# Kernel optimization log

Hardware: AMD Instinct MI355X
Metric: run time of the kernel (lower is better)

## Reference

```python
import jax, jax.numpy as jnp
import numpy as np

B, L, D, H, K = 4, 4096, 1024, 16, 256

def setup_inputs() -> dict:
    key = jax.random.key(0)
    ks = jax.random.split(key, 11)
    s = 0.02
    return {
        "x": jax.random.normal(ks[0], (B, L, D), jnp.float32),
        "Wq": jax.random.normal(ks[1], (D, D), jnp.float32) * s,
        "bq": jax.random.normal(ks[2], (D,), jnp.float32) * s,
        "Wk": jax.random.normal(ks[3], (D, D), jnp.float32) * s,
        "bk": jax.random.normal(ks[4], (D,), jnp.float32) * s,
        "Wv": jax.random.normal(ks[5], (D, D), jnp.float32) * s,
        "bv": jax.random.normal(ks[6], (D,), jnp.float32) * s,
        "E": jax.random.normal(ks[7], (L, K), jnp.float32),
        "F": jax.random.normal(ks[8], (L, K), jnp.float32),
        "Wo": jax.random.normal(ks[9], (D, D), jnp.float32) * s,
        "bo": jax.random.normal(ks[10], (D,), jnp.float32) * s,
        "n_heads": H,
    }

def reference(x, Wq, bq, Wk, bk, Wv, bv, E, F, Wo, bo, n_heads):
    Bc, Lc, Dc = x.shape
    hd = Dc // n_heads
    scale = hd ** -0.5
    # QKV projections (torch Linear: x @ W.T + b; here W stored as [in,out])
    q = (x @ Wq + bq).reshape(Bc, Lc, n_heads, hd)  # blhd
    k = (x @ Wk + bk).reshape(Bc, Lc, n_heads, hd)
    v = (x @ Wv + bv).reshape(Bc, Lc, n_heads, hd)
    # Low-rank projection of K/V sequence dim: L -> K
    kE = jnp.einsum('blhd,lk->bhkd', k, E[:Lc])
    vF = jnp.einsum('blhd,lk->bhkd', v, F[:Lc])
    # Attention over compressed dim k
    qk = jnp.einsum('blhd,bhkd->bhlk', q, kE) * scale
    attn = jax.nn.softmax(qk, axis=-1)
    out = jnp.einsum('bhlk,bhkd->blhd', attn, vF).reshape(Bc, Lc, Dc)
    return out @ Wo + bo
```

## Files before the change

kernel.cpp:

```cpp
#include <hip/hip_runtime.h>

typedef _Float16 half_t;
typedef __attribute__((ext_vector_type(8))) _Float16 f16x8;
typedef __attribute__((ext_vector_type(4))) _Float16 f16x4;
typedef __attribute__((ext_vector_type(4))) float f32x4;
typedef __attribute__((ext_vector_type(4))) float float4v;

__device__ __forceinline__ void gload_lds16(const void* g, void* l) {
  __builtin_amdgcn_global_load_lds(
      (const __attribute__((address_space(1))) void*)g,
      (__attribute__((address_space(3))) void*)l, 16, 0, 0);
}

template<int OUTMODE>
__global__ __launch_bounds__(512, 2)
void gemm_big(const half_t* __restrict__ A, const half_t* __restrict__ Bt,
              void* __restrict__ Cv, const float* __restrict__ bias, float alpha)
{
  __shared__ __attribute__((aligned(16))) char lds[131072];
  const int tid = threadIdx.x, w = tid >> 6, lane = tid & 63;
  const int wr = w >> 2, wc = w & 3;
  const int g = lane >> 4, cc = lane & 15;
  const int m0 = blockIdx.x * 256, n0 = blockIdx.y * 256;

  const int srow2 = tid >> 2, sslot = tid & 3;
  const int swslot = sslot ^ ((srow2 >> 1) & 3);
  const int swr = (g ^ ((cc >> 1) & 3)) << 4;

  const f32x4 zero = {0.f, 0.f, 0.f, 0.f};
  f32x4 acc[8][4];
#pragma unroll
  for (int i = 0; i < 8; ++i)
#pragma unroll
    for (int j = 0; j < 4; ++j) acc[i][j] = zero;

  auto STAGE_HALF = [&](int ktile, int hh, char* sb) {
    const int kk = hh >> 1, isB = hh & 1;
    const half_t* src = isB ? Bt : A;
    const int base_row = isB ? n0 : m0;
    const long rowoff = (long)(base_row + srow2) * 1024 + ktile * 64 + kk * 32 + swslot * 8;
    char* d = sb + isB * 32768 + kk * 16384;
    gload_lds16(src + rowoff,          d + tid * 16);
    gload_lds16(src + rowoff + 131072, d + 8192 + tid * 16);
  };

  {
    char* b0 = lds;
    STAGE_HALF(0, 0, b0); STAGE_HALF(0, 1, b0);
    STAGE_HALF(0, 2, b0); STAGE_HALF(0, 3, b0);
  }
  asm volatile("s_waitcnt vmcnt(4)" ::: "memory");
  __builtin_amdgcn_s_barrier();

#pragma unroll 1
  for (int n = 0; n < 16; ++n) {
    const char* rb = lds + ((n & 1) << 16);
    char* sb = lds + (((n + 1) & 1) << 16);
    f16x8 bf[4];
#pragma unroll
    for (int ph = 0; ph < 4; ++ph) {
      const int kk = ph >> 1, fh = ph & 1;
      f16x8 af[4];
      const char* Ah = rb + kk * 16384;
#pragma unroll
      for (int mf = 0; mf < 4; ++mf)
        af[mf] = *(const f16x8*)(Ah + (wr * 128 + fh * 64 + mf * 16 + cc) * 64 + swr);
      if (fh == 0) {
        const char* Bh = rb + 32768 + kk * 16384;
#pragma unroll
        for (int nf = 0; nf < 4; ++nf)
          bf[nf] = *(const f16x8*)(Bh + (wc * 64 + nf * 16 + cc) * 64 + swr);
      }
      if (n < 15) STAGE_HALF(n + 1, ph, sb);
      __builtin_amdgcn_sched_barrier(0);
      __builtin_amdgcn_s_barrier();
      asm volatile("s_waitcnt lgkmcnt(0)" ::: "memory");
      __builtin_amdgcn_sched_barrier(0);
      __builtin_amdgcn_s_setprio(1);
#pragma unroll
      for (int mf = 0; mf < 4; ++mf)
#pragma unroll
        for (int nf = 0; nf < 4; ++nf)
          acc[fh * 4 + mf][nf] =
              __builtin_amdgcn_mfma_f32_16x16x32_f16(af[mf], bf[nf], acc[fh * 4 + mf][nf], 0, 0, 0);
      __builtin_amdgcn_s_setprio(0);
      __builtin_amdgcn_sched_barrier(0);
      if (ph == 1) {
        if (n < 15) { asm volatile("s_waitcnt vmcnt(4)" ::: "memory"); }
        else        { asm volatile("s_waitcnt vmcnt(0)" ::: "memory"); }
      } else if (ph == 3) {
        if (n < 15) { asm volatile("s_waitcnt vmcnt(4)" ::: "memory"); }
      }
      __builtin_amdgcn_s_barrier();
    }
  }

#pragma unroll
  for (int mf = 0; mf < 8; ++mf)
#pragma unroll
    for (int nf = 0; nf < 4; ++nf)
#pragma unroll
      for (int r = 0; r < 4; ++r) {
        const int row = m0 + wr * 128 + mf * 16 + g * 4 + r;
        const int col = n0 + wc * 64 + nf * 16 + cc;
        float v = (acc[mf][nf][r] + bias[col]) * alpha;
        if (OUTMODE == 0) {
          ((float*)Cv)[(long)row * 1024 + col] = v;
        } else if (OUTMODE == 1) {
          ((half_t*)Cv)[(long)row * 1024 + col] = (half_t)v;
        } else {
          const int bb = row >> 12, l = row & 4095, h = col >> 6, d = col & 63;
          ((half_t*)Cv)[(((long)(bb * 16 + h) * 4096 + l) << 6) + d] = (half_t)v;
        }
      }
}

template<int BM, int BN, int WM, int WN, int OUTF16, int MODE, int SK>
__global__ __launch_bounds__(256, 2)
void gemm_bt(const half_t* __restrict__ A, const half_t* __restrict__ Bt,
             void* __restrict__ Cv, const float* __restrict__ bias,
             const float* __restrict__ rowscale,
             int M, int N, int K, int lda, int ldb, int ldc, float alpha,
             long sA, long sB, long sC)
{
  constexpr int FM = WM / 16, FN = WN / 16, CW = BN / WN;
  __shared__ __attribute__((aligned(16))) half_t As[BM * 32];
  __shared__ __attribute__((aligned(16))) half_t Bs[BN * 32];

  const int tid = threadIdx.x, w = tid >> 6, lane = tid & 63;
  const int wr = w / CW, wc = w % CW;
  const int z = blockIdx.z / SK, ks = blockIdx.z % SK;
  const half_t* Ab = A + (long)z * sA;
  const half_t* Bb = Bt + (long)z * sB;
  const int m0 = blockIdx.x * BM, n0 = blockIdx.y * BN;
  const int g = lane >> 4, cc = lane & 15;
  const int srow = lane >> 2, scol = (lane & 3) * 8;

  const f32x4 zero = {0.f, 0.f, 0.f, 0.f};
  f32x4 acc[FM][FN];
#pragma unroll
  for (int i = 0; i < FM; ++i)
#pragma unroll
    for (int j = 0; j < FN; ++j) acc[i][j] = zero;

  const int kchunk = K / SK;
  for (int kt = ks * kchunk; kt < (ks + 1) * kchunk; kt += 32) {
#pragma unroll
    for (int j = 0; j < BM / 64; ++j) {
      const int bi = w * (BM / 64) + j;
      gload_lds16(Ab + (long)(m0 + bi * 16 + srow) * lda + kt + scol, &As[bi * 512]);
    }
#pragma unroll
    for (int j = 0; j < BN / 64; ++j) {
      const int bi = w * (BN / 64) + j;
      gload_lds16(Bb + (long)(n0 + bi * 16 + srow) * ldb + kt + scol, &Bs[bi * 512]);
    }
    __syncthreads();

    f16x8 af[FM], bf[FN];
#pragma unroll
    for (int i = 0; i < FM; ++i)
      af[i] = *(const f16x8*)&As[(wr * WM + i * 16 + cc) * 32 + g * 8];
#pragma unroll
    for (int j = 0; j < FN; ++j)
      bf[j] = *(const f16x8*)&Bs[(wc * WN + j * 16 + cc) * 32 + g * 8];
#pragma unroll
    for (int i = 0; i < FM; ++i)
#pragma unroll
      for (int j = 0; j < FN; ++j)
        acc[i][j] = __builtin_amdgcn_mfma_f32_16x16x32_f16(af[i], bf[j], acc[i][j], 0, 0, 0);
    __syncthreads();
  }

  const long coff = (long)z * sC;
#pragma unroll
  for (int i = 0; i < FM; ++i)
#pragma unroll
    for (int j = 0; j < FN; ++j)
#pragma unroll
      for (int r = 0; r < 4; ++r) {
        const int row = m0 + wr * WM + i * 16 + g * 4 + r;
        const int col = n0 + wc * WN + j * 16 + cc;
        float v = acc[i][j][r];
        if (MODE == 1) v = (v + bias[col]) * alpha;
        if (MODE == 2 || MODE == 4) v = v + rowscale[row] * bias[col];
        if (MODE == 3) {
          const int nb = gridDim.z / SK;
          ((float*)Cv)[((long)ks * nb + z) * sC + (long)row * ldc + col] = v;
        } else if (MODE == 4) {
          ((half_t*)Cv)[coff + (long)(col >> 6) * ((long)M * 64) + (long)row * 64 + (col & 63)]
              = (half_t)v;
        } else {
          if (OUTF16) ((half_t*)Cv)[coff + (long)row * ldc + col] = (half_t)v;
          else        ((float*)Cv)[coff + (long)row * ldc + col] = v;
        }
      }
}

__global__ __launch_bounds__(512, 2)
void attn_fused(const half_t* __restrict__ qhb, const half_t* __restrict__ kEh,
                const half_t* __restrict__ vFt, half_t* __restrict__ outp, int L)
{
  __shared__ __attribute__((aligned(16))) half_t Ks[256 * 64];
  __shared__ __attribute__((aligned(16))) half_t Vs[64 * 256];
  const int tid = threadIdx.x, w = tid >> 6, lane = tid & 63;
  const int g = lane >> 4, c = lane & 15;
  const int l0 = blockIdx.x * 256, h = blockIdx.y, b = blockIdx.z;

  const half_t* keh = kEh + (long)(b * 16 + h) * 16384;
  const half_t* vfh = vFt + (long)b * 262144 + (long)h * 16384;
  const half_t* qpan = qhb + ((long)(b * 16 + h) * 4096 + l0) * 64;
  half_t* ob = outp + ((long)b * L + l0 + w * 32) * 1024 + h * 64;

#pragma unroll
  for (int i = 0; i < 4; ++i) {
    const int row = i * 64 + (tid >> 3), slot = tid & 7;
    gload_lds16(qpan + row * 64 + ((slot ^ (row & 7)) << 3),
                (char*)Ks + i * 8192 + tid * 16);
  }
  __syncthreads();

  f16x8 qf[2][2];
#pragma unroll
  for (int fi = 0; fi < 2; ++fi) {
    const int qrow = w * 32 + fi * 16 + c;
    const char* qp = (const char*)Ks + qrow * 128;
#pragma unroll
    for (int ks = 0; ks < 2; ++ks)
      qf[fi][ks] = *(const f16x8*)(qp + (((ks * 4 + g) ^ (qrow & 7)) << 4));
  }
  __syncthreads();

#pragma unroll
  for (int i = 0; i < 4; ++i) {
    const int row = i * 64 + (tid >> 3), slot = tid & 7;
    gload_lds16(keh + row * 64 + ((slot ^ (row & 7)) << 3),
                (char*)Ks + i * 8192 + tid * 16);
  }
#pragma unroll
  for (int i = 0; i < 4; ++i) {
    const int row = i * 16 + (tid >> 5), slot = tid & 31;
    gload_lds16(vfh + row * 256 + ((slot ^ (row & 7)) << 3),
                (char*)Vs + i * 8192 + tid * 16);
  }
  __syncthreads();

  const f32x4 zero = {0.f, 0.f, 0.f, 0.f};
  f32x4 o[2][4];
#pragma unroll
  for (int fi = 0; fi < 2; ++fi)
#pragma unroll
    for (int fd = 0; fd < 4; ++fd) o[fi][fd] = zero;
  float mrun[2] = {-3.0e38f, -3.0e38f};
  float lrun[2] = {0.f, 0.f};

  for (int ch = 0; ch < 4; ++ch) {
    f32x4 s[2][4];
#pragma unroll
    for (int fi = 0; fi < 2; ++fi)
#pragma unroll
      for (int fj = 0; fj < 4; ++fj) s[fi][fj] = zero;
#pragma unroll
    for (int fj = 0; fj < 4; ++fj) {
      const int krow = ch * 64 + fj * 16 + c;
      const char* kb = (const char*)Ks + krow * 128;
      f16x8 k0 = *(const f16x8*)(kb + ((g ^ (c & 7)) << 4));
      f16x8 k1 = *(const f16x8*)(kb + (((4 + g) ^ (c & 7)) << 4));
#pragma unroll
      for (int fi = 0; fi < 2; ++fi) {
        s[fi][fj] = __builtin_amdgcn_mfma_f32_16x16x32_f16(k0, qf[fi][0], s[fi][fj], 0, 0, 0);
        s[fi][fj] = __builtin_amdgcn_mfma_f32_16x16x32_f16(k1, qf[fi][1], s[fi][fj], 0, 0, 0);
      }
    }

    f16x4 p[2][4];
#pragma unroll
    for (int fi = 0; fi < 2; ++fi) {
      float cm = -3.0e38f;
#pragma unroll
      for (int fj = 0; fj < 4; ++fj)
#pragma unroll
        for (int r = 0; r < 4; ++r) cm = fmaxf(cm, s[fi][fj][r]);
      cm = fmaxf(cm, __shfl_xor(cm, 16));
      cm = fmaxf(cm, __shfl_xor(cm, 32));
      const float mnew = fmaxf(mrun[fi], cm);
      const float sc = __expf(mrun[fi] - mnew);
      float csum = 0.f;
#pragma unroll
      for (int fj = 0; fj < 4; ++fj) {
        f16x4 fr;
#pragma unroll
        for (int r = 0; r < 4; ++r) {
          float e = __expf(s[fi][fj][r] - mnew);
          fr[r] = (half_t)e; csum += e;
        }
        p[fi][fj] = fr;
      }
      csum += __shfl_xor(csum, 16);
      csum += __shfl_xor(csum, 32);
      lrun[fi] = lrun[fi] * sc + csum;
      mrun[fi] = mnew;
#pragma unroll
      for (int fd = 0; fd < 4; ++fd)
#pragma unroll
        for (int r = 0; r < 4; ++r) o[fi][fd][r] *= sc;
    }

#pragma unroll
    for (int kc = 0; kc < 4; ++kc) {
      const int s16 = ch * 8 + kc * 2 + (g >> 1);
      f16x4 va[4];
#pragma unroll
      for (int fd = 0; fd < 4; ++fd) {
        const int drow = fd * 16 + c;
        va[fd] = *(const f16x4*)((const char*)Vs + drow * 512 +
                                 ((s16 ^ (c & 7)) << 4) + (g & 1) * 8);
      }
#pragma unroll
      for (int fi = 0; fi < 2; ++fi)
#pragma unroll
        for (int fd = 0; fd < 4; ++fd)
          o[fi][fd] = __builtin_amdgcn_mfma_f32_16x16x16f16(va[fd], p[fi][kc], o[fi][fd], 0, 0, 0);
    }
  }

#pragma unroll
  for (int fi = 0; fi < 2; ++fi) {
    const float inv = 1.0f / lrun[fi];
#pragma unroll
    for (int fd = 0; fd < 4; ++fd) {
      f16x4 st;
#pragma unroll
      for (int r = 0; r < 4; ++r) st[r] = (half_t)(o[fi][fd][r] * inv);
      *(f16x4*)(ob + (long)(fi * 16 + c) * 1024 + fd * 16 + g * 4) = st;
    }
  }
}

__global__ void reduce4_f16(const float* __restrict__ in, half_t* __restrict__ out) {
  long i = ((long)blockIdx.x * 256 + threadIdx.x) * 4;
  float4v a = *(const float4v*)(in + i);
#pragma unroll
  for (int ks = 1; ks < 4; ++ks) {
    float4v t = *(const float4v*)(in + (long)ks * 2097152 + i);
    a.x += t.x; a.y += t.y; a.z += t.z; a.w += t.w;
  }
  f16x4 o;
  o[0] = (half_t)a.x; o[1] = (half_t)a.y; o[2] = (half_t)a.z; o[3] = (half_t)a.w;
  *(f16x4*)(out + i) = o;
}

__global__ void xpass(const float* __restrict__ x, half_t* __restrict__ xhf,
                      half_t* __restrict__ xT) {
  __shared__ float t[32][33];
  const int b = blockIdx.z, d0 = blockIdx.x * 32, l0 = blockIdx.y * 32;
  const int tx = threadIdx.x, ty = threadIdx.y;
  const float* ip = x + ((long)b * 4096 + l0) * 1024 + d0;
  half_t* oh = xhf + ((long)b * 4096 + l0) * 1024 + d0;
#pragma unroll
  for (int j = 0; j < 4; ++j) {
    float v = ip[(long)(ty + 8 * j) * 1024 + tx];
    t[ty + 8 * j][tx] = v;
    oh[(long)(ty + 8 * j) * 1024 + tx] = (half_t)v;
  }
  __syncthreads();
  half_t* ot = xT + ((long)b * 1024 + d0) * 4096 + l0;
#pragma unroll
  for (int j = 0; j < 4; ++j)
    ot[(long)(ty + 8 * j) * 4096 + tx] = (half_t)t[tx][ty + 8 * j];
}

__global__ void efpass(const float* __restrict__ E, const float* __restrict__ F,
                       half_t* __restrict__ outT, float* __restrict__ ssum) {
  __shared__ float t[32][33];
  __shared__ float ps[8][32];
  const int zz = blockIdx.z;
  const float* in = zz ? F : E;
  half_t* oT = outT + (long)zz * 1048576;
  float* sm = ssum + zz * 256;
  const int k0 = blockIdx.x * 32, l0 = blockIdx.y * 32;
  const int tx = threadIdx.x, ty = threadIdx.y;
  float p = 0.f;
#pragma unroll
  for (int j = 0; j < 4; ++j) {
    float v = in[(long)(l0 + ty + 8 * j) * 256 + k0 + tx];
    t[ty + 8 * j][tx] = v; p += v;
  }
  ps[ty][tx] = p;
  __syncthreads();
  if (ty == 0) {
    float a = 0.f;
#pragma unroll
    for (int r = 0; r < 8; ++r) a += ps[r][tx];
    atomicAdd(&sm[k0 + tx], a);
  }
#pragma unroll
  for (int j = 0; j < 4; ++j)
    oT[(long)(k0 + ty + 8 * j) * 4096 + l0 + tx] = (half_t)t[tx][ty + 8 * j];
}

__global__ void transposeW(const float* __restrict__ W0, const float* __restrict__ W1,
                           const float* __restrict__ W2, const float* __restrict__ W3,
                           half_t* __restrict__ out0, half_t* __restrict__ out1,
                           half_t* __restrict__ out2, half_t* __restrict__ out3) {
  __shared__ float t[32][33];
  const int zz = blockIdx.z;
  const float* in = (zz == 0) ? W0 : (zz == 1) ? W1 : (zz == 2) ? W2 : W3;
  half_t* out = (zz == 0) ? out0 : (zz == 1) ? out1 : (zz == 2) ? out2 : out3;
  const int cx = blockIdx.x * 32 + threadIdx.x;
  const int r0 = blockIdx.y * 32;
#pragma unroll
  for (int j = 0; j < 4; ++j)
    t[threadIdx.y + 8 * j][threadIdx.x] = in[(long)(r0 + threadIdx.y + 8 * j) * 1024 + cx];
  __syncthreads();
  const int rx = r0 + threadIdx.x;
  const int cy = blockIdx.x * 32 + threadIdx.y;
#pragma unroll
  for (int j = 0; j < 4; ++j)
    out[(long)(cy + 8 * j) * 1024 + rx] = (half_t)t[threadIdx.x][threadIdx.y + 8 * j];
}

extern "C" void kernel_launch(void* const* d_in, const int* in_sizes, int n_in,
                              void* d_out, int out_size, void* d_ws, size_t ws_size,
                              hipStream_t stream)
{
  const float* x  = (const float*)d_in[0];
  const float* Wq = (const float*)d_in[1];
  const float* bq = (const float*)d_in[2];
  const float* Wk = (const float*)d_in[3];
  const float* bk = (const float*)d_in[4];
  const float* Wv = (const float*)d_in[5];
  const float* bv = (const float*)d_in[6];
  const float* E  = (const float*)d_in[7];
  const float* F  = (const float*)d_in[8];
  const float* Wo = (const float*)d_in[9];
  const float* bo = (const float*)d_in[10];
  float* out = (float*)d_out;

  char* ws = (char*)d_ws;
  half_t* xhf  = (half_t*)(ws);
  half_t* xT   = (half_t*)(ws + 33554432);
  half_t* qhf  = (half_t*)(ws + 67108864);
  half_t* Wqt  = (half_t*)(ws + 100663296);
  half_t* Wkt  = Wqt + 1048576;
  half_t* Wvt  = Wkt + 1048576;
  half_t* Wot  = Wvt + 1048576;
  half_t* EFt  = (half_t*)(ws + 109051904);
  half_t* xEF  = (half_t*)(ws + 113246208);
  half_t* kEb  = (half_t*)(ws + 117440512);
  half_t* vFtb = (half_t*)(ws + 119537664);
  float*  sEF  = (float*)(ws + 121634816);
  half_t* outp = xhf;
  float*  xEFf = (float*)d_out;

  hipMemsetAsync(sEF, 0, 2048, stream);
  dim3 tb(32, 8);
  xpass<<<dim3(32, 128, 4), tb, 0, stream>>>(x, xhf, xT);
  efpass<<<dim3(8, 128, 2), tb, 0, stream>>>(E, F, EFt, sEF);
  transposeW<<<dim3(32, 32, 4), tb, 0, stream>>>(Wq, Wk, Wv, Wo, Wqt, Wkt, Wvt, Wot);

  gemm_bt<128,128,64,64,0,3,4><<<dim3(4, 8, 16), 256, 0, stream>>>(
      EFt, xT, (void*)xEFf, nullptr, nullptr, 512, 1024, 4096, 4096, 4096, 1024, 1.f,
      0, 4194304, 524288);
  reduce4_f16<<<2048, 256, 0, stream>>>(xEFf, xEF);

  gemm_big<2><<<dim3(64, 4), 512, 0, stream>>>(xhf, Wqt, qhf, bq, 0.125f);
  gemm_bt<64,64,32,32,1,4,1><<<dim3(4, 16, 4), 256, 0, stream>>>(
      xEF, Wkt, kEb, bk, sEF, 256, 1024, 1024, 1024, 1024, 1024, 1.f,
      524288, 0, 262144);
  gemm_bt<64,64,32,32,1,2,1><<<dim3(16, 4, 4), 256, 0, stream>>>(
      Wvt, xEF + 262144, vFtb, sEF + 256, bv, 1024, 256, 1024, 1024, 1024, 256, 1.f,
      0, 524288, 262144);
  attn_fused<<<dim3(16, 16, 4), 512, 0, stream>>>(qhf, kEb, vFtb, outp, 4096);
  gemm_big<0><<<dim3(64, 4), 512, 0, stream>>>(outp, Wot, (void*)out, bo, 1.0f);
  (void)in_sizes; (void)n_in; (void)out_size; (void)ws_size;
}
```

Before: 226.5 us.

## Merge prep and kE/vF kernels, hoist V load, skip softmax rescales

Merges the three preprocessing kernels (x transpose/convert, E/F transpose with column sums, weight transposes) into one launch. Merges the kE and vF projection GEMMs into one launch split by block role, and specializes the xEF GEMM. In attention, the V tile load is issued alongside the Q load so it overlaps the Q fragment extraction. The online softmax now skips rescaling when every lane's new max stays within 8 of the running max. Fewer launches and less rescale work are traded for branchy kernels and a looser softmax reference max that could raise overflow risk in fp32 exp sums.

```diff
diff --git a/kernel.cpp b/kernel.cpp
--- a/kernel.cpp
+++ b/kernel.cpp
@@ -106,8 +106,6 @@
         float v = (acc[mf][nf][r] + bias[col]) * alpha;
         if (OUTMODE == 0) {
           ((float*)Cv)[(long)row * 1024 + col] = v;
-        } else if (OUTMODE == 1) {
-          ((half_t*)Cv)[(long)row * 1024 + col] = (half_t)v;
         } else {
           const int bb = row >> 12, l = row & 4095, h = col >> 6, d = col & 63;
           ((half_t*)Cv)[(((long)(bb * 16 + h) * 4096 + l) << 6) + d] = (half_t)v;
@@ -115,84 +113,135 @@
       }
 }
 
-template<int BM, int BN, int WM, int WN, int OUTF16, int MODE, int SK>
+template<int SK>
 __global__ __launch_bounds__(256, 2)
-void gemm_bt(const half_t* __restrict__ A, const half_t* __restrict__ Bt,
-             void* __restrict__ Cv, const float* __restrict__ bias,
-             const float* __restrict__ rowscale,
-             int M, int N, int K, int lda, int ldb, int ldc, float alpha,
-             long sA, long sB, long sC)
+void gemm_xef(const half_t* __restrict__ A, const half_t* __restrict__ Bt,
+              float* __restrict__ Cv, int lda, int ldb, long sB, long sC)
 {
-  constexpr int FM = WM / 16, FN = WN / 16, CW = BN / WN;
-  __shared__ __attribute__((aligned(16))) half_t As[BM * 32];
-  __shared__ __attribute__((aligned(16))) half_t Bs[BN * 32];
+  __shared__ __attribute__((aligned(16))) half_t As[128 * 32];
+  __shared__ __attribute__((aligned(16))) half_t Bs[128 * 32];
 
   const int tid = threadIdx.x, w = tid >> 6, lane = tid & 63;
-  const int wr = w / CW, wc = w % CW;
+  const int wr = w >> 1, wc = w & 1;
   const int z = blockIdx.z / SK, ks = blockIdx.z % SK;
-  const half_t* Ab = A + (long)z * sA;
+  const half_t* Ab = A;
   const half_t* Bb = Bt + (long)z * sB;
-  const int m0 = blockIdx.x * BM, n0 = blockIdx.y * BN;
+  const int m0 = blockIdx.x * 128, n0 = blockIdx.y * 128;
   const int g = lane >> 4, cc = lane & 15;
   const int srow = lane >> 2, scol = (lane & 3) * 8;
 
   const f32x4 zero = {0.f, 0.f, 0.f, 0.f};
-  f32x4 acc[FM][FN];
-#pragma unroll
-  for (int i = 0; i < FM; ++i)
-#pragma unroll
-    for (int j = 0; j < FN; ++j) acc[i][j] = zero;
-
-  const int kchunk = K / SK;
+  f32x4 acc[4][4];
+#pragma unroll
+  for (int i = 0; i < 4; ++i)
+#pragma unroll
+    for (int j = 0; j < 4; ++j) acc[i][j] = zero;
+
+  const int kchunk = 4096 / SK;
   for (int kt = ks * kchunk; kt < (ks + 1) * kchunk; kt += 32) {
 #pragma unroll
-    for (int j = 0; j < BM / 64; ++j) {
-      const int bi = w * (BM / 64) + j;
+    for (int j = 0; j < 2; ++j) {
+      const int bi = w * 2 + j;
       gload_lds16(Ab + (long)(m0 + bi * 16 + srow) * lda + kt + scol, &As[bi * 512]);
-    }
-#pragma unroll
-    for (int j = 0; j < BN / 64; ++j) {
-      const int bi = w * (BN / 64) + j;
       gload_lds16(Bb + (long)(n0 + bi * 16 + srow) * ldb + kt + scol, &Bs[bi * 512]);
     }
     __syncthreads();
 
-    f16x8 af[FM], bf[FN];
-#pragma unroll
-    for (int i = 0; i < FM; ++i)
-      af[i] = *(const f16x8*)&As[(wr * WM + i * 16 + cc) * 32 + g * 8];
-#pragma unroll
-    for (int j = 0; j < FN; ++j)
-      bf[j] = *(const f16x8*)&Bs[(wc * WN + j * 16 + cc) * 32 + g * 8];
-#pragma unroll
-    for (int i = 0; i < FM; ++i)
-#pragma unroll
-      for (int j = 0; j < FN; ++j)
+    f16x8 af[4], bf[4];
+#pragma unroll
+    for (int i = 0; i < 4; ++i)
+      af[i] = *(const f16x8*)&As[(wr * 64 + i * 16 + cc) * 32 + g * 8];
+#pragma unroll
+    for (int j = 0; j < 4; ++j)
+      bf[j] = *(const f16x8*)&Bs[(wc * 64 + j * 16 + cc) * 32 + g * 8];
+#pragma unroll
+    for (int i = 0; i < 4; ++i)
+#pragma unroll
+      for (int j = 0; j < 4; ++j)
         acc[i][j] = __builtin_amdgcn_mfma_f32_16x16x32_f16(af[i], bf[j], acc[i][j], 0, 0, 0);
     __syncthreads();
   }
 
-  const long coff = (long)z * sC;
-#pragma unroll
-  for (int i = 0; i < FM; ++i)
-#pragma unroll
-    for (int j = 0; j < FN; ++j)
+  const int nb = gridDim.z / SK;
+#pragma unroll
+  for (int i = 0; i < 4; ++i)
+#pragma unroll
+    for (int j = 0; j < 4; ++j)
 #pragma unroll
       for (int r = 0; r < 4; ++r) {
-        const int row = m0 + wr * WM + i * 16 + g * 4 + r;
-        const int col = n0 + wc * WN + j * 16 + cc;
+        const int row = m0 + wr * 64 + i * 16 + g * 4 + r;
+        const int col = n0 + wc * 64 + j * 16 + cc;
+        Cv[((long)ks * nb + z) * sC + (long)row * 1024 + col] = acc[i][j][r];
+      }
+}
+
+__global__ __launch_bounds__(256, 2)
+void gemm_kevf(const half_t* __restrict__ xEF, const half_t* __restrict__ Wkt,
+               const half_t* __restrict__ Wvt, half_t* __restrict__ kEb,
+               half_t* __restrict__ vFtb, const float* __restrict__ bk,
+               const float* __restrict__ bv, const float* __restrict__ sEF)
+{
+  __shared__ __attribute__((aligned(16))) half_t As[64 * 32];
+  __shared__ __attribute__((aligned(16))) half_t Bs[64 * 32];
+  const int tid = threadIdx.x, w = tid >> 6, lane = tid & 63;
+  const int wr = w >> 1, wc = w & 1;
+  const int g = lane >> 4, cc = lane & 15;
+  const int srow = lane >> 2, scol = (lane & 3) * 8;
+
+  const int bid = blockIdx.x;
+  const int role = bid >> 8, lb = bid & 255;
+  const half_t *Ap, *Bp;
+  int m0, n0, z;
+  if (role == 0) {
+    m0 = (lb & 3) * 64; n0 = ((lb >> 2) & 15) * 64; z = lb >> 6;
+    Ap = xEF + (long)z * 524288;  Bp = Wkt;
+  } else {
+    m0 = (lb & 15) * 64; n0 = ((lb >> 4) & 3) * 64; z = lb >> 6;
+    Ap = Wvt;  Bp = xEF + (long)z * 524288 + 262144;
+  }
+
+  const f32x4 zero = {0.f, 0.f, 0.f, 0.f};
+  f32x4 acc[2][2];
+#pragma unroll
+  for (int i = 0; i < 2; ++i)
+#pragma unroll
+    for (int j = 0; j < 2; ++j) acc[i][j] = zero;
+
+  for (int kt = 0; kt < 1024; kt += 32) {
+    gload_lds16(Ap + (long)(m0 + w * 16 + srow) * 1024 + kt + scol, &As[w * 512]);
+    gload_lds16(Bp + (long)(n0 + w * 16 + srow) * 1024 + kt + scol, &Bs[w * 512]);
+    __syncthreads();
+    f16x8 af[2], bf[2];
+#pragma unroll
+    for (int i = 0; i < 2; ++i)
+      af[i] = *(const f16x8*)&As[(wr * 32 + i * 16 + cc) * 32 + g * 8];
+#pragma unroll
+    for (int j = 0; j < 2; ++j)
+      bf[j] = *(const f16x8*)&Bs[(wc * 32 + j * 16 + cc) * 32 + g * 8];
+#pragma unroll
+    for (int i = 0; i < 2; ++i)
+#pragma unroll
+      for (int j = 0; j < 2; ++j)
+        acc[i][j] = __builtin_amdgcn_mfma_f32_16x16x32_f16(af[i], bf[j], acc[i][j], 0, 0, 0);
+    __syncthreads();
+  }
+
+#pragma unroll
+  for (int i = 0; i < 2; ++i)
+#pragma unroll
+    for (int j = 0; j < 2; ++j)
+#pragma unroll
+      for (int r = 0; r < 4; ++r) {
+        const int row = m0 + wr * 32 + i * 16 + g * 4 + r;
+        const int col = n0 + wc * 32 + j * 16 + cc;
         float v = acc[i][j][r];
-        if (MODE == 1) v = (v + bias[col]) * alpha;
-        if (MODE == 2 || MODE == 4) v = v + rowscale[row] * bias[col];
-        if (MODE == 3) {
-          const int nb = gridDim.z / SK;
-          ((float*)Cv)[((long)ks * nb + z) * sC + (long)row * ldc + col] = v;
-        } else if (MODE == 4) {
-          ((half_t*)Cv)[coff + (long)(col >> 6) * ((long)M * 64) + (long)row * 64 + (col & 63)]
+        if (role == 0) {
+          v += sEF[row] * bk[col];
+          kEb[(long)z * 262144 + (long)(col >> 6) * 16384 + (long)row * 64 + (col & 63)]
               = (half_t)v;
         } else {
-          if (OUTF16) ((half_t*)Cv)[coff + (long)row * ldc + col] = (half_t)v;
-          else        ((float*)Cv)[coff + (long)row * ldc + col] = v;
+          v += bv[row] * sEF[256 + col];
+          vFtb[(long)z * 262144 + (long)row * 256 + col] = (half_t)v;
         }
       }
 }
@@ -218,6 +267,12 @@
     gload_lds16(qpan + row * 64 + ((slot ^ (row & 7)) << 3),
                 (char*)Ks + i * 8192 + tid * 16);
   }
+#pragma unroll
+  for (int i = 0; i < 4; ++i) {
+    const int row = i * 16 + (tid >> 5), slot = tid & 31;
+    gload_lds16(vfh + row * 256 + ((slot ^ (row & 7)) << 3),
+                (char*)Vs + i * 8192 + tid * 16);
+  }
   __syncthreads();
 
   f16x8 qf[2][2];
@@ -236,12 +291,6 @@
     const int row = i * 64 + (tid >> 3), slot = tid & 7;
     gload_lds16(keh + row * 64 + ((slot ^ (row & 7)) << 3),
                 (char*)Ks + i * 8192 + tid * 16);
-  }
-#pragma unroll
-  for (int i = 0; i < 4; ++i) {
-    const int row = i * 16 + (tid >> 5), slot = tid & 31;
-    gload_lds16(vfh + row * 256 + ((slot ^ (row & 7)) << 3),
-                (char*)Vs + i * 8192 + tid * 16);
   }
   __syncthreads();
 
@@ -283,8 +332,9 @@
         for (int r = 0; r < 4; ++r) cm = fmaxf(cm, s[fi][fj][r]);
       cm = fmaxf(cm, __shfl_xor(cm, 16));
       cm = fmaxf(cm, __shfl_xor(cm, 32));
-      const float mnew = fmaxf(mrun[fi], cm);
-      const float sc = __expf(mrun[fi] - mnew);
+      const float mref = mrun[fi];
+      const bool keep = __all(cm - mref <= 8.0f);
+      const float mnew = keep ? mref : fmaxf(mref, cm);
       float csum = 0.f;
 #pragma unroll
       for (int fj = 0; fj < 4; ++fj) {
@@ -298,12 +348,17 @@
       }
       csum += __shfl_xor(csum, 16);
       csum += __shfl_xor(csum, 32);
-      lrun[fi] = lrun[fi] * sc + csum;
-      mrun[fi] = mnew;
-#pragma unroll
-      for (int fd = 0; fd < 4; ++fd)
-#pragma unroll
-        for (int r = 0; r < 4; ++r) o[fi][fd][r] *= sc;
+      if (keep) {
+        lrun[fi] += csum;
+      } else {
+        const float sc = __expf(mref - mnew);
+        lrun[fi] = lrun[fi] * sc + csum;
+        mrun[fi] = mnew;
+#pragma unroll
+        for (int fd = 0; fd < 4; ++fd)
+#pragma unroll
+          for (int r = 0; r < 4; ++r) o[fi][fd][r] *= sc;
+      }
     }
 
 #pragma unroll
@@ -337,6 +392,78 @@
   }
 }
 
+__global__ __launch_bounds__(256, 4)
+void prepass(const float* __restrict__ x, half_t* __restrict__ xhf,
+             half_t* __restrict__ xT,
+             const float* __restrict__ E, const float* __restrict__ F,
+             half_t* __restrict__ EFt, float* __restrict__ sEF,
+             const float* __restrict__ Wq, const float* __restrict__ Wk,
+             const float* __restrict__ Wv, const float* __restrict__ Wo,
+             half_t* __restrict__ Wqt, half_t* __restrict__ Wkt,
+             half_t* __restrict__ Wvt, half_t* __restrict__ Wot)
+{
+  __shared__ float t[32][33];
+  __shared__ float ps[8][32];
+  const int tx = threadIdx.x, ty = threadIdx.y;
+  const int id = blockIdx.x;
+
+  if (id < 16384) {
+    const int bx = id & 31, by = (id >> 5) & 127, bz = id >> 12;
+    const int d0 = bx * 32, l0 = by * 32;
+    const float* ip = x + ((long)bz * 4096 + l0) * 1024 + d0;
+    half_t* oh = xhf + ((long)bz * 4096 + l0) * 1024 + d0;
+#pragma unroll
+    for (int j = 0; j < 4; ++j) {
+      float v = ip[(long)(ty + 8 * j) * 1024 + tx];
+      t[ty + 8 * j][tx] = v;
+      oh[(long)(ty + 8 * j) * 1024 + tx] = (half_t)v;
+    }
+    __syncthreads();
+    half_t* ot = xT + ((long)bz * 1024 + d0) * 4096 + l0;
+#pragma unroll
+    for (int j = 0; j < 4; ++j)
+      ot[(long)(ty + 8 * j) * 4096 + tx] = (half_t)t[tx][ty + 8 * j];
+  } else if (id < 18432) {
+    const int id2 = id - 16384;
+    const int bx = id2 & 7, by = (id2 >> 3) & 127, zz = id2 >> 10;
+    const float* in = zz ? F : E;
+    half_t* oT = EFt + (long)zz * 1048576;
+    float* sm = sEF + zz * 256;
+    const int k0 = bx * 32, l0 = by * 32;
+    float p = 0.f;
+#pragma unroll
+    for (int j = 0; j < 4; ++j) {
+      float v = in[(long)(l0 + ty + 8 * j) * 256 + k0 + tx];
+      t[ty + 8 * j][tx] = v; p += v;
+    }
+    ps[ty][tx] = p;
+    __syncthreads();
+    if (ty == 0) {
+      float a = 0.f;
+#pragma unroll
+      for (int r = 0; r < 8; ++r) a += ps[r][tx];
+      atomicAdd(&sm[k0 + tx], a);
+    }
+#pragma unroll
+    for (int j = 0; j < 4; ++j)
+      oT[(long)(k0 + ty + 8 * j) * 4096 + l0 + tx] = (half_t)t[tx][ty + 8 * j];
+  } else {
+    const int id3 = id - 18432;
+    const int bx = id3 & 31, by = (id3 >> 5) & 31, zz = id3 >> 10;
+    const float* in = (zz == 0) ? Wq : (zz == 1) ? Wk : (zz == 2) ? Wv : Wo;
+    half_t* out = (zz == 0) ? Wqt : (zz == 1) ? Wkt : (zz == 2) ? Wvt : Wot;
+    const int cx = bx * 32 + tx, r0 = by * 32;
+#pragma unroll
+    for (int j = 0; j < 4; ++j)
+      t[ty + 8 * j][tx] = in[(long)(r0 + ty + 8 * j) * 1024 + cx];
+    __syncthreads();
+    const int rx = r0 + tx, cy = bx * 32 + ty;
+#pragma unroll
+    for (int j = 0; j < 4; ++j)
+      out[(long)(cy + 8 * j) * 1024 + rx] = (half_t)t[tx][ty + 8 * j];
+  }
+}
+
 __global__ void reduce4_f16(const float* __restrict__ in, half_t* __restrict__ out) {
   long i = ((long)blockIdx.x * 256 + threadIdx.x) * 4;
   float4v a = *(const float4v*)(in + i);
@@ -348,76 +475,6 @@
   f16x4 o;
   o[0] = (half_t)a.x; o[1] = (half_t)a.y; o[2] = (half_t)a.z; o[3] = (half_t)a.w;
   *(f16x4*)(out + i) = o;
-}
-
-__global__ void xpass(const float* __restrict__ x, half_t* __restrict__ xhf,
-                      half_t* __restrict__ xT) {
-  __shared__ float t[32][33];
-  const int b = blockIdx.z, d0 = blockIdx.x * 32, l0 = blockIdx.y * 32;
-  const int tx = threadIdx.x, ty = threadIdx.y;
-  const float* ip = x + ((long)b * 4096 + l0) * 1024 + d0;
-  half_t* oh = xhf + ((long)b * 4096 + l0) * 1024 + d0;
-#pragma unroll
-  for (int j = 0; j < 4; ++j) {
-    float v = ip[(long)(ty + 8 * j) * 1024 + tx];
-    t[ty + 8 * j][tx] = v;
-    oh[(long)(ty + 8 * j) * 1024 + tx] = (half_t)v;
-  }
-  __syncthreads();
-  half_t* ot = xT + ((long)b * 1024 + d0) * 4096 + l0;
-#pragma unroll
-  for (int j = 0; j < 4; ++j)
-    ot[(long)(ty + 8 * j) * 4096 + tx] = (half_t)t[tx][ty + 8 * j];
-}
-
-__global__ void efpass(const float* __restrict__ E, const float* __restrict__ F,
-                       half_t* __restrict__ outT, float* __restrict__ ssum) {
-  __shared__ float t[32][33];
-  __shared__ float ps[8][32];
-  const int zz = blockIdx.z;
-  const float* in = zz ? F : E;
-  half_t* oT = outT + (long)zz * 1048576;
-  float* sm = ssum + zz * 256;
-  const int k0 = blockIdx.x * 32, l0 = blockIdx.y * 32;
-  const int tx = threadIdx.x, ty = threadIdx.y;
-  float p = 0.f;
-#pragma unroll
-  for (int j = 0; j < 4; ++j) {
-    float v = in[(long)(l0 + ty + 8 * j) * 256 + k0 + tx];
-    t[ty + 8 * j][tx] = v; p += v;
-  }
-  ps[ty][tx] = p;
-  __syncthreads();
-  if (ty == 0) {
-    float a = 0.f;
-#pragma unroll
-    for (int r = 0; r < 8; ++r) a += ps[r][tx];
-    atomicAdd(&sm[k0 + tx], a);
-  }
-#pragma unroll
-  for (int j = 0; j < 4; ++j)
-    oT[(long)(k0 + ty + 8 * j) * 4096 + l0 + tx] = (half_t)t[tx][ty + 8 * j];
-}
-
-__global__ void transposeW(const float* __restrict__ W0, const float* __restrict__ W1,
-                           const float* __restrict__ W2, const float* __restrict__ W3,
-                           half_t* __restrict__ out0, half_t* __restrict__ out1,
-                           half_t* __restrict__ out2, half_t* __restrict__ out3) {
-  __shared__ float t[32][33];
-  const int zz = blockIdx.z;
-  const float* in = (zz == 0) ? W0 : (zz == 1) ? W1 : (zz == 2) ? W2 : W3;
-  half_t* out = (zz == 0) ? out0 : (zz == 1) ? out1 : (zz == 2) ? out2 : out3;
-  const int cx = blockIdx.x * 32 + threadIdx.x;
-  const int r0 = blockIdx.y * 32;
-#pragma unroll
-  for (int j = 0; j < 4; ++j)
-    t[threadIdx.y + 8 * j][threadIdx.x] = in[(long)(r0 + threadIdx.y + 8 * j) * 1024 + cx];
-  __syncthreads();
-  const int rx = r0 + threadIdx.x;
-  const int cy = blockIdx.x * 32 + threadIdx.y;
-#pragma unroll
-  for (int j = 0; j < 4; ++j)
-    out[(long)(cy + 8 * j) * 1024 + rx] = (half_t)t[threadIdx.x][threadIdx.y + 8 * j];
 }
 
 extern "C" void kernel_launch(void* const* d_in, const int* in_sizes, int n_in,
@@ -454,24 +511,16 @@
   float*  xEFf = (float*)d_out;
 
   hipMemsetAsync(sEF, 0, 2048, stream);
-  dim3 tb(32, 8);
-  xpass<<<dim3(32, 128, 4), tb, 0, stream>>>(x, xhf, xT);
-  efpass<<<dim3(8, 128, 2), tb, 0, stream>>>(E, F, EFt, sEF);
-  transposeW<<<dim3(32, 32, 4), tb, 0, stream>>>(Wq, Wk, Wv, Wo, Wqt, Wkt, Wvt, Wot);
-
-  gemm_bt<128,128,64,64,0,3,4><<<dim3(4, 8, 16), 256, 0, stream>>>(
-      EFt, xT, (void*)xEFf, nullptr, nullptr, 512, 1024, 4096, 4096, 4096, 1024, 1.f,
-      0, 4194304, 524288);
+  prepass<<<dim3(22528), dim3(32, 8), 0, stream>>>(
+      x, xhf, xT, E, F, EFt, sEF, Wq, Wk, Wv, Wo, Wqt, Wkt, Wvt, Wot);
+
+  gemm_xef<4><<<dim3(4, 8, 16), 256, 0, stream>>>(
+      EFt, xT, xEFf, 4096, 4096, 4194304, 524288);
   reduce4_f16<<<2048, 256, 0, stream>>>(xEFf, xEF);
 
   gemm_big<2><<<dim3(64, 4), 512, 0, stream>>>(xhf, Wqt, qhf, bq, 0.125f);
-  gemm_bt<64,64,32,32,1,4,1><<<dim3(4, 16, 4), 256, 0, stream>>>(
-      xEF, Wkt, kEb, bk, sEF, 256, 1024, 1024, 1024, 1024, 1024, 1.f,
-      524288, 0, 262144);
-  gemm_bt<64,64,32,32,1,2,1><<<dim3(16, 4, 4), 256, 0, stream>>>(
-      Wvt, xEF + 262144, vFtb, sEF + 256, bv, 1024, 256, 1024, 1024, 1024, 256, 1.f,
-      0, 524288, 262144);
+  gemm_kevf<<<dim3(512), 256, 0, stream>>>(xEF, Wkt, Wvt, kEb, vFtb, bk, bv, sEF);
   attn_fused<<<dim3(16, 16, 4), 512, 0, stream>>>(qhf, kEb, vFtb, outp, 4096);
   gemm_big<0><<<dim3(64, 4), 512, 0, stream>>>(outp, Wot, (void*)out, bo, 1.0f);
-  (void)in_sizes; (void)n_in; (void)out_size; (void)ws_size;
-}
+  (void)bq; (void)in_sizes; (void)n_in; (void)out_size; (void)ws_size;
+}
```

Result: faster. 216.4 us (-4.5%).
